# Optimization experiments

Hardware: AMD Instinct MI355X
Metric: run time of the kernel (lower is better)

Reference implementation:

```python
import jax, jax.numpy as jnp
import numpy as np
from jax import lax

CLAMP = 4.135
OUT = 7            # RoI pool output size
SCALE = 1.0 / 16.0 # feature-map stride 16


def bilinear_gather(feat, bidx, y, x):
    """feat [B,C,H,W]; bidx [N] int; y,x [N,Ph,Pw] coords in feature space -> [N,C,Ph,Pw]."""
    B, C, H, W = feat.shape
    y = jnp.clip(y, 0.0, H - 1.0)
    x = jnp.clip(x, 0.0, W - 1.0)
    y0 = jnp.floor(y); x0 = jnp.floor(x)
    y0i = y0.astype(jnp.int32); x0i = x0.astype(jnp.int32)
    y1i = jnp.minimum(y0i + 1, H - 1); x1i = jnp.minimum(x0i + 1, W - 1)
    wy1 = y - y0; wx1 = x - x0
    wy0 = 1.0 - wy1; wx0 = 1.0 - wx1
    flat = feat.transpose(0, 2, 3, 1).reshape(B * H * W, C)
    base = (bidx * (H * W))[:, None, None]
    def g(yy, xx):
        return flat[base + yy * W + xx]  # [N,Ph,Pw,C]
    out = ((wy0 * wx0)[..., None] * g(y0i, x0i)
           + (wy0 * wx1)[..., None] * g(y0i, x1i)
           + (wy1 * wx0)[..., None] * g(y1i, x0i)
           + (wy1 * wx1)[..., None] * g(y1i, x1i))
    return out.transpose(0, 3, 1, 2)


def roi_align(feat, boxes, bidx):
    """RoIAlign, sampling_ratio=1 (one bilinear sample per bin center)."""
    N = boxes.shape[0]
    b = boxes * SCALE
    x1, y1, x2, y2 = b[:, 0], b[:, 1], b[:, 2], b[:, 3]
    bw = jnp.maximum(x2 - x1, 1.0) / OUT
    bh = jnp.maximum(y2 - y1, 1.0) / OUT
    c = jnp.arange(OUT, dtype=feat.dtype) + 0.5
    ys = y1[:, None] + c * bh[:, None]   # [N,OUT]
    xs = x1[:, None] + c * bw[:, None]
    yg = jnp.broadcast_to(ys[:, :, None], (N, OUT, OUT))
    xg = jnp.broadcast_to(xs[:, None, :], (N, OUT, OUT))
    return bilinear_gather(feat, bidx, yg, xg)


def xyxy_to_rbox(b):
    cx = (b[:, 0] + b[:, 2]) * 0.5
    cy = (b[:, 1] + b[:, 3]) * 0.5
    w = b[:, 2] - b[:, 0]
    h = b[:, 3] - b[:, 1]
    return jnp.stack([cx, cy, w, h, jnp.zeros_like(cx)], axis=1)


def decode_deltas_to_rboxes(rboxes, deltas):
    cx, cy, w, h, a = (rboxes[:, i] for i in range(5))
    dx, dy, dw, dh, da = (deltas[:, i] for i in range(5))
    return jnp.stack([cx + dx * w, cy + dy * h,
                      w * jnp.exp(dw), h * jnp.exp(dh), a + da], axis=1)


def grid_sample_zeros(feat, gx, gy):
    """F.grid_sample(bilinear, padding_mode='zeros', align_corners=False).
    feat [N,C,H,W]; gx,gy [N,Ho,Wo] normalized coords -> [N,C,Ho,Wo]."""
    N, C, H, W = feat.shape
    ix = ((gx + 1.0) * W - 1.0) * 0.5
    iy = ((gy + 1.0) * H - 1.0) * 0.5
    x0 = jnp.floor(ix); y0 = jnp.floor(iy)
    wx1 = ix - x0; wy1 = iy - y0
    x0i = x0.astype(jnp.int32); y0i = y0.astype(jnp.int32)
    flat = feat.transpose(0, 2, 3, 1).reshape(N, H * W, C)
    Ho, Wo = gx.shape[1], gx.shape[2]
    def g(yy, xx, wt):
        valid = ((yy >= 0) & (yy < H) & (xx >= 0) & (xx < W)).astype(feat.dtype)
        idx = jnp.clip(yy, 0, H - 1) * W + jnp.clip(xx, 0, W - 1)
        v = jnp.take_along_axis(flat, idx.reshape(N, -1, 1), axis=1)
        v = v.reshape(N, Ho, Wo, C)
        return (wt * valid)[..., None] * v
    out = (g(y0i, x0i, (1 - wy1) * (1 - wx1))
           + g(y0i, x0i + 1, (1 - wy1) * wx1)
           + g(y0i + 1, x0i, wy1 * (1 - wx1))
           + g(y0i + 1, x0i + 1, wy1 * wx1))
    return out.transpose(0, 3, 1, 2)


def setup_inputs() -> dict:
    key = jax.random.key(0)
    ks = jax.random.split(key, 12)
    B, C, H, W = 2, 256, 64, 64
    N, NC = 2048, 16
    FD = C * OUT * OUT  # 12544
    features = jax.random.normal(ks[0], (B, C, H, W), jnp.float32)
    # valid image-space boxes (image 1024x1024, stride-16 features)
    cx = jax.random.uniform(ks[1], (N,), minval=96.0, maxval=928.0)
    cy = jax.random.uniform(ks[2], (N,), minval=96.0, maxval=928.0)
    bw = jax.random.uniform(ks[3], (N,), minval=16.0, maxval=128.0)
    bh = jax.random.uniform(ks[4], (N,), minval=16.0, maxval=128.0)
    proposals = jnp.stack([cx - bw / 2, cy - bh / 2, cx + bw / 2, cy + bh / 2], axis=1)
    batch_idx = jnp.repeat(jnp.arange(B, dtype=jnp.int32), N // B)
    s = 0.02
    return {
        "features": features,
        "proposals": proposals,
        "batch_idx": batch_idx,
        "conv_w": jax.random.normal(ks[5], (C, C, 3, 3), jnp.float32) * s,
        "conv_b": jnp.zeros((C,), jnp.float32),
        "align_w": jax.random.normal(ks[6], (5, FD), jnp.float32) * s,
        "align_b": jnp.zeros((5,), jnp.float32),
        "fc1_w": jax.random.normal(ks[7], (1024, FD), jnp.float32) * s,
        "fc1_b": jnp.zeros((1024,), jnp.float32),
        "fc2_w": jax.random.normal(ks[8], (1024, 1024), jnp.float32) * s,
        "fc2_b": jnp.zeros((1024,), jnp.float32),
        "cls_w": jax.random.normal(ks[9], (NC, 1024), jnp.float32) * s,
        "cls_b": jnp.zeros((NC,), jnp.float32),
        "box_w": jax.random.normal(ks[10], (5, 1024), jnp.float32) * s,
        "box_b": jnp.zeros((5,), jnp.float32),
    }


def reference(features, proposals, batch_idx, conv_w, conv_b, align_w, align_b,
              fc1_w, fc1_b, fc2_w, fc2_b, cls_w, cls_b, box_w, box_b):
    N = proposals.shape[0]
    # 1) RoI align
    box_feat = roi_align(features, proposals, batch_idx)           # [N,256,7,7]
    a = lax.conv_general_dilated(box_feat, conv_w, (1, 1), ((1, 1), (1, 1)),
                                 dimension_numbers=("NCHW", "OIHW", "NCHW"))
    a = jax.nn.relu(a + conv_b[None, :, None, None]).reshape(N, -1)
    coarse = jnp.clip(a @ align_w.T + align_b, -CLAMP, CLAMP)      # [N,5]
    # 3) decode to rboxes (torch.no_grad -> stop_gradient)
    prop_rb = xyxy_to_rbox(proposals)
    align_rb = lax.stop_gradient(decode_deltas_to_rboxes(prop_rb, coarse))
    # 4) affine grid from rbox (no translation, matches source) + grid_sample
    w, h, ang = align_rb[:, 2], align_rb[:, 3], align_rb[:, 4]
    cth, sth = jnp.cos(ang), jnp.sin(ang)
    sx, sy = w / OUT, h / OUT
    base = (2.0 * jnp.arange(OUT, dtype=box_feat.dtype) + 1.0) / OUT - 1.0
    xb = base[None, None, :]
    yb = base[None, :, None]
    gx = (sx * cth)[:, None, None] * xb + (-(sy * sth))[:, None, None] * yb
    gy = (sx * sth)[:, None, None] * xb + (sy * cth)[:, None, None] * yb
    aligned = grid_sample_zeros(box_feat, gx, gy)                  # [N,256,7,7]
    # 5) refine head MLP + predictors
    r = jax.nn.relu(aligned.reshape(N, -1) @ fc1_w.T + fc1_b)
    r = jax.nn.relu(r @ fc2_w.T + fc2_b)
    logits = r @ cls_w.T + cls_b                                   # [N,16]
    final = jnp.clip(r @ box_w.T + box_b, -CLAMP, CLAMP)           # [N,5]
    # 6) eval-path decode + softmax (per-class NMS is dynamic-shape postproc, excluded)
    pred_rboxes = decode_deltas_to_rboxes(prop_rb, final)
    scores = jax.nn.softmax(logits, axis=-1)
    return jnp.concatenate([pred_rboxes, scores], axis=1)          # [N,21]
```

## Files before the change

### kernel.cpp

```cpp
#include <hip/hip_runtime.h>
#include <hip/hip_bf16.h>
#include <math.h>
#include <type_traits>

constexpr int B = 2, C = 256, H = 64, W = 64, HW = H * W;
constexpr int N = 2048, OUT = 7, P = 49, FD = C * P;
constexpr int K1 = 1024;
constexpr float CLAMP_V = 4.135f, SCALE_V = 1.0f / 16.0f;
constexpr int LDB = 264;

typedef short s8v __attribute__((ext_vector_type(8)));
typedef short s4v __attribute__((ext_vector_type(4)));
typedef float f32x4 __attribute__((ext_vector_type(4)));

template <int I, int NN, class F>
__device__ __forceinline__ void static_for(F&& f) {
    if constexpr (I < NN) {
        f(std::integral_constant<int, I>{});
        static_for<I + 1, NN>(static_cast<F&&>(f));
    }
}

__device__ __forceinline__ int xcd_swz(int blk, int nblk) {
    const int cpx = nblk >> 3;
    return (blk & 7) * cpx + (blk >> 3);
}

__global__ void k_prep_all(const float* __restrict__ features, float* __restrict__ featT,
                           const float* __restrict__ conv_w, __hip_bfloat16* __restrict__ wB,
                           const float* __restrict__ align_w, float4* __restrict__ aw4,
                           float* __restrict__ aw1,
                           const float* __restrict__ fc1_w, __hip_bfloat16* __restrict__ fc1B,
                           const float* __restrict__ fc2_w, __hip_bfloat16* __restrict__ fc2B) {
    __shared__ float smem[64 * 49];
    const int id = blockIdx.x;
    const int t = threadIdx.x;
    if (id < 2048) {
        const int x = id % 128, y = (id / 128) % 8, b = id / 1024;
        const int c0 = y * 32, p0 = x * 32;
        const int tx = t % 32, ty = t / 32;
        float* tile = smem;
#pragma unroll
        for (int r = 0; r < 32; r += 8)
            tile[(ty + r) * 33 + tx] = features[(size_t)(b * C + c0 + ty + r) * HW + p0 + tx];
        __syncthreads();
#pragma unroll
        for (int r = 0; r < 32; r += 8)
            featT[(size_t)(b * HW + p0 + ty + r) * C + c0 + tx] = tile[tx * 33 + ty + r];
    } else if (id < 2120) {
        const int T = id - 2048;
        const int tap = T / 8, s = T % 8;
        const int co = t;
#pragma unroll
        for (int q = 0; q < 4; ++q)
#pragma unroll
            for (int j = 0; j < 8; ++j) {
                const int ci = s * 32 + q * 8 + j;
                wB[(((size_t)T * 256 + co) * 4 + q) * 8 + j] =
                    __float2bfloat16(conv_w[(size_t)co * 2304 + ci * 9 + tap]);
            }
    } else if (id < 2169) {
        const int o = id - 2120;
        const int co = t;
        float4 v;
        v.x = align_w[(size_t)0 * FD + co * 49 + o];
        v.y = align_w[(size_t)1 * FD + co * 49 + o];
        v.z = align_w[(size_t)2 * FD + co * 49 + o];
        v.w = align_w[(size_t)3 * FD + co * 49 + o];
        aw4[o * 256 + co] = v;
        aw1[o * 256 + co] = align_w[(size_t)4 * FD + co * 49 + o];
    } else if (id < 6265) {
        const int q = id - 2169;
        const int c0 = (q % 4) * 64;
        const int o = q / 4;
        const float* src = fc1_w + (size_t)o * FD + (size_t)c0 * 49;
        for (int i = t; i < 64 * 49; i += 256) smem[i] = src[i];
        __syncthreads();
        __hip_bfloat16* dst = fc1B + (size_t)o * FD + c0;
        for (int j = t; j < 64 * 49; j += 256) {
            const int p = j >> 6, cc = j & 63;
            dst[(size_t)p * 256 + cc] = __float2bfloat16(smem[cc * 49 + p]);
        }
    } else {
        const int bid = id - 6265;
        const int n4 = (K1 * K1) / 4;
        for (int i = bid * 256 + t; i < n4; i += 256 * 256) {
            const float4 v = reinterpret_cast<const float4*>(fc2_w)[i];
            fc2B[i * 4 + 0] = __float2bfloat16(v.x);
            fc2B[i * 4 + 1] = __float2bfloat16(v.y);
            fc2B[i * 4 + 2] = __float2bfloat16(v.z);
            fc2B[i * 4 + 3] = __float2bfloat16(v.w);
        }
    }
}

__global__ __launch_bounds__(256, 2) void k_roi_conv_grid(
    const float* __restrict__ featT, const float* __restrict__ proposals,
    const int* __restrict__ bidx, const __hip_bfloat16* __restrict__ wB,
    const float* __restrict__ conv_b, const float4* __restrict__ aw4,
    const float* __restrict__ aw1, const float* __restrict__ align_b,
    __hip_bfloat16* __restrict__ alignedOut) {
    __shared__ __align__(16) __hip_bfloat16 bfh[100 * LDB];
    __shared__ float red[64];

    const int blk = xcd_swz(blockIdx.x, 1024);
    const int t = threadIdx.x;
    const int lane = t & 63, wid = t >> 6;
    const int l15 = lane & 15;
    const int qofs = (lane >> 4) * 8;

#pragma unroll
    for (int r = 0; r < 2; ++r) {
        const int n = blk * 2 + r;
        const float px1 = proposals[n * 4 + 0] * SCALE_V, py1 = proposals[n * 4 + 1] * SCALE_V;
        const float px2 = proposals[n * 4 + 2] * SCALE_V, py2 = proposals[n * 4 + 3] * SCALE_V;
        const float bw = fmaxf(px2 - px1, 1.0f) * (1.0f / OUT);
        const float bh = fmaxf(py2 - py1, 1.0f) * (1.0f / OUT);
        const int b = bidx[n];
        const float* fb = featT + (size_t)b * HW * C;
        for (int p = wid; p < P; p += 4) {
            const int pyi = p / 7, pxi = p % 7;
            float y = py1 + (pyi + 0.5f) * bh;
            float x = px1 + (pxi + 0.5f) * bw;
            y = fminf(fmaxf(y, 0.f), (float)(H - 1));
            x = fminf(fmaxf(x, 0.f), (float)(W - 1));
            const float y0f = floorf(y), x0f = floorf(x);
            const int y0 = (int)y0f, x0 = (int)x0f;
            const int y1 = min(y0 + 1, H - 1), x1 = min(x0 + 1, W - 1);
            const float wy1 = y - y0f, wx1 = x - x0f;
            const float wy0 = 1.f - wy1, wx0 = 1.f - wx1;
            const int c4 = lane * 4;
            const float4 v00 = *reinterpret_cast<const float4*>(&fb[(size_t)(y0 * W + x0) * C + c4]);
            const float4 v01 = *reinterpret_cast<const float4*>(&fb[(size_t)(y0 * W + x1) * C + c4]);
            const float4 v10 = *reinterpret_cast<const float4*>(&fb[(size_t)(y1 * W + x0) * C + c4]);
            const float4 v11 = *reinterpret_cast<const float4*>(&fb[(size_t)(y1 * W + x1) * C + c4]);
            s4v o4;
            o4[0] = (short)__bfloat16_as_ushort(__float2bfloat16(
                        wy0 * (wx0 * v00.x + wx1 * v01.x) + wy1 * (wx0 * v10.x + wx1 * v11.x)));
            o4[1] = (short)__bfloat16_as_ushort(__float2bfloat16(
                        wy0 * (wx0 * v00.y + wx1 * v01.y) + wy1 * (wx0 * v10.y + wx1 * v11.y)));
            o4[2] = (short)__bfloat16_as_ushort(__float2bfloat16(
                        wy0 * (wx0 * v00.z + wx1 * v01.z) + wy1 * (wx0 * v10.z + wx1 * v11.z)));
            o4[3] = (short)__bfloat16_as_ushort(__float2bfloat16(
                        wy0 * (wx0 * v00.w + wx1 * v01.w) + wy1 * (wx0 * v10.w + wx1 * v11.w)));
            *reinterpret_cast<s4v*>(&bfh[(2 * p + r) * LDB + c4]) = o4;
        }
    }
    bfh[98 * LDB + t] = __float2bfloat16(0.f);
    bfh[99 * LDB + t] = __float2bfloat16(0.f);
    __syncthreads();

    const int rp = l15 & 1;
    int oyt[7], oxt[7];
    bool pval[7];
    static_for<0, 7>([&](auto MT) {
        const int p = (MT.value * 16 + l15) >> 1;
        pval[MT.value] = (p < 49);
        oyt[MT.value] = p / 7;
        oxt[MT.value] = p % 7;
    });
    int bofs[4];
    static_for<0, 4>([&](auto NT) {
        const int col = wid * 64 + NT.value * 16 + l15;
        bofs[NT.value] = col * 32 + qofs;
    });

    f32x4 acc[7][4] = {};
    for (int tap = 0; tap < 9; ++tap) {
        const int dy = tap / 3 - 1, dx = tap % 3 - 1;
        int rsel[7];
        static_for<0, 7>([&](auto MT) {
            const int iy = oyt[MT.value] + dy, ix = oxt[MT.value] + dx;
            const bool v = pval[MT.value] && ((unsigned)iy < 7u) && ((unsigned)ix < 7u);
            rsel[MT.value] = (v ? (2 * (iy * 7 + ix) + rp) : (98 + rp)) * LDB;
        });
        const __hip_bfloat16* wTap = wB + (size_t)tap * 8 * 8192;
#pragma unroll
        for (int s = 0; s < 8; ++s) {
            s8v af[7], bfr[4];
            static_for<0, 4>([&](auto NT) {
                bfr[NT.value] = *reinterpret_cast<const s8v*>(&wTap[(size_t)s * 8192 + bofs[NT.value]]);
            });
            static_for<0, 7>([&](auto MT) {
                af[MT.value] = *reinterpret_cast<const s8v*>(&bfh[rsel[MT.value] + s * 32 + qofs]);
            });
            __builtin_amdgcn_s_setprio(1);
            static_for<0, 7>([&](auto MT) {
                static_for<0, 4>([&](auto NT) {
                    acc[MT.value][NT.value] = __builtin_amdgcn_mfma_f32_16x16x32_bf16(
                        af[MT.value], bfr[NT.value], acc[MT.value][NT.value], 0, 0, 0);
                });
            });
            __builtin_amdgcn_s_setprio(0);
        }
    }

    const int hi = lane >> 4;
    float cb[4];
    static_for<0, 4>([&](auto NT) { cb[NT.value] = conv_b[wid * 64 + NT.value * 16 + l15]; });
    float pc[2][5] = {};
    static_for<0, 7>([&](auto MT) {
        static_for<0, 4>([&](auto RR) {
            constexpr int r = RR.value & 1;
            const int p = MT.value * 8 + hi * 2 + (RR.value >> 1);
            if (p < 49) {
                static_for<0, 4>([&](auto NT) {
                    const int co = wid * 64 + NT.value * 16 + l15;
                    const float4 w4 = aw4[p * 256 + co];
                    const float  w1 = aw1[p * 256 + co];
                    const float a = fmaxf(acc[MT.value][NT.value][RR.value] + cb[NT.value], 0.f);
                    pc[r][0] = fmaf(a, w4.x, pc[r][0]);
                    pc[r][1] = fmaf(a, w4.y, pc[r][1]);
                    pc[r][2] = fmaf(a, w4.z, pc[r][2]);
                    pc[r][3] = fmaf(a, w4.w, pc[r][3]);
                    pc[r][4] = fmaf(a, w1,   pc[r][4]);
                });
            }
        });
    });
    static_for<0, 2>([&](auto RI) {
        static_for<0, 5>([&](auto J) {
            float s = pc[RI.value][J.value];
#pragma unroll
            for (int off = 32; off; off >>= 1) s += __shfl_xor(s, off);
            pc[RI.value][J.value] = s;
        });
        if (lane == 0) {
            static_for<0, 5>([&](auto J) { red[RI.value * 20 + wid * 5 + J.value] = pc[RI.value][J.value]; });
        }
    });
    __syncthreads();

    if (t < 2) {
        const int r = t;
        const int n = blk * 2 + r;
        float coarse[5];
        static_for<0, 5>([&](auto Jc) {
            constexpr int j = Jc.value;
            float s = red[r * 20 + j] + red[r * 20 + 5 + j] + red[r * 20 + 10 + j] +
                      red[r * 20 + 15 + j] + align_b[j];
            coarse[j] = fminf(fmaxf(s, -CLAMP_V), CLAMP_V);
        });
        const float x1r = proposals[n * 4 + 0], y1r = proposals[n * 4 + 1];
        const float x2r = proposals[n * 4 + 2], y2r = proposals[n * 4 + 3];
        const float w = x2r - x1r, h = y2r - y1r;
        const float w2 = w * expf(coarse[2]);
        const float h2 = h * expf(coarse[3]);
        const float ang = coarse[4];
        const float cth = cosf(ang), sth = sinf(ang);
        const float sx = w2 * (1.0f / OUT), sy = h2 * (1.0f / OUT);
        red[48 + r * 4 + 0] = sx * cth;
        red[48 + r * 4 + 1] = sy * sth;
        red[48 + r * 4 + 2] = sx * sth;
        red[48 + r * 4 + 3] = sy * cth;
    }
    __syncthreads();

#pragma unroll
    for (int r = 0; r < 2; ++r) {
        const float gA = red[48 + r * 4 + 0], gBv = red[48 + r * 4 + 1];
        const float gC = red[48 + r * 4 + 2], gD = red[48 + r * 4 + 3];
        __hip_bfloat16* ao = alignedOut + (size_t)(blk * 2 + r) * FD;
        const int c4 = lane * 4;
        for (int p = wid; p < P; p += 4) {
            const int pyi = p / 7, pxi = p % 7;
            const float xb = (2 * pxi + 1) * (1.0f / OUT) - 1.0f;
            const float yb = (2 * pyi + 1) * (1.0f / OUT) - 1.0f;
            const float gx = gA * xb - gBv * yb;
            const float gy = gC * xb + gD * yb;
            const float ix = ((gx + 1.0f) * OUT - 1.0f) * 0.5f;
            const float iy = ((gy + 1.0f) * OUT - 1.0f) * 0.5f;
            const float x0f = floorf(ix), y0f = floorf(iy);
            const int x0 = (int)x0f, y0 = (int)y0f;
            const float wx1 = ix - x0f, wy1 = iy - y0f;
            const float wx0 = 1.f - wx1, wy0 = 1.f - wy1;
            const float w00 = wy0 * wx0, w01 = wy0 * wx1, w10 = wy1 * wx0, w11 = wy1 * wx1;
            const bool vx0 = (unsigned)x0 < 7u, vx1 = (unsigned)(x0 + 1) < 7u;
            const bool vy0 = (unsigned)y0 < 7u, vy1 = (unsigned)(y0 + 1) < 7u;
            const int r00 = (vy0 && vx0) ? (y0 * 7 + x0) : 49;
            const int r01 = (vy0 && vx1) ? (y0 * 7 + x0 + 1) : 49;
            const int r10 = (vy1 && vx0) ? ((y0 + 1) * 7 + x0) : 49;
            const int r11 = (vy1 && vx1) ? ((y0 + 1) * 7 + x0 + 1) : 49;
            const s4v b00 = *reinterpret_cast<const s4v*>(&bfh[(2 * r00 + r) * LDB + c4]);
            const s4v b01 = *reinterpret_cast<const s4v*>(&bfh[(2 * r01 + r) * LDB + c4]);
            const s4v b10 = *reinterpret_cast<const s4v*>(&bfh[(2 * r10 + r) * LDB + c4]);
            const s4v b11 = *reinterpret_cast<const s4v*>(&bfh[(2 * r11 + r) * LDB + c4]);
            s4v o4;
            static_for<0, 4>([&](auto J) {
                constexpr int j = J.value;
                float v = w00 * __bfloat162float(__ushort_as_bfloat16((unsigned short)b00[j]))
                        + w01 * __bfloat162float(__ushort_as_bfloat16((unsigned short)b01[j]))
                        + w10 * __bfloat162float(__ushort_as_bfloat16((unsigned short)b10[j]))
                        + w11 * __bfloat162float(__ushort_as_bfloat16((unsigned short)b11[j]));
                o4[j] = (short)__bfloat16_as_ushort(__float2bfloat16(v));
            });
            *reinterpret_cast<s4v*>(&ao[p * 256 + c4]) = o4;
        }
    }
}

template <int BM, int BN, int BK>
__global__ __launch_bounds__(256, 4) void k_gemm_bf16(
    const __hip_bfloat16* __restrict__ A, const __hip_bfloat16* __restrict__ Wt,
    const float* __restrict__ bias, float* __restrict__ CoutF,
    __hip_bfloat16* __restrict__ CoutH, int M, int Nn, int K, int relu) {
    constexpr int LD = BK + 8;
    __shared__ __align__(16) __hip_bfloat16 As[2][BM * LD];
    __shared__ __align__(16) __hip_bfloat16 Ws[2][BN * LD];
    const int ntb = Nn / BN;
    const int blkS = xcd_swz(blockIdx.x, gridDim.x);
    const int bx = blkS % ntb, by = blkS / ntb;
    const int t = threadIdx.x;
    const int lane = t & 63, wid = t >> 6;
    const int l15 = lane & 15;
    const int qofs = (lane >> 4) * 8;
    const int wm = wid >> 1, wn = wid & 1;

    const int ar = t >> 3, ak = (t & 7) * 8;
    const size_t aBase = (size_t)(by * BM) * K;
    const size_t bBase = (size_t)(bx * BN) * K;

    f32x4 acc[2][2] = {};

    const int steps = K / BK;
    {
        const s8v a0 = *reinterpret_cast<const s8v*>(&A[aBase + (size_t)ar * K + ak]);
        const s8v a1 = *reinterpret_cast<const s8v*>(&A[aBase + (size_t)(ar + 32) * K + ak]);
        const s8v b0 = *reinterpret_cast<const s8v*>(&Wt[bBase + (size_t)ar * K + ak]);
        const s8v b1 = *reinterpret_cast<const s8v*>(&Wt[bBase + (size_t)(ar + 32) * K + ak]);
        *reinterpret_cast<s8v*>(&As[0][ar * LD + ak]) = a0;
        *reinterpret_cast<s8v*>(&As[0][(ar + 32) * LD + ak]) = a1;
        *reinterpret_cast<s8v*>(&Ws[0][ar * LD + ak]) = b0;
        *reinterpret_cast<s8v*>(&Ws[0][(ar + 32) * LD + ak]) = b1;
    }
    __syncthreads();

    for (int s = 0; s < steps; ++s) {
        const int cur = s & 1;
        const bool pf = (s + 1 < steps);
        s8v a0, a1, b0, b1;
        if (pf) {
            const int k0 = (s + 1) * BK;
            a0 = *reinterpret_cast<const s8v*>(&A[aBase + (size_t)ar * K + k0 + ak]);
            a1 = *reinterpret_cast<const s8v*>(&A[aBase + (size_t)(ar + 32) * K + k0 + ak]);
            b0 = *reinterpret_cast<const s8v*>(&Wt[bBase + (size_t)ar * K + k0 + ak]);
            b1 = *reinterpret_cast<const s8v*>(&Wt[bBase + (size_t)(ar + 32) * K + k0 + ak]);
        }
        static_for<0, 2>([&](auto KH) {
            s8v afr[2], bfr[2];
            static_for<0, 2>([&](auto MT) {
                afr[MT.value] = *reinterpret_cast<const s8v*>(
                    &As[cur][(wm * 32 + MT.value * 16 + l15) * LD + KH.value * 32 + qofs]);
            });
            static_for<0, 2>([&](auto NT) {
                bfr[NT.value] = *reinterpret_cast<const s8v*>(
                    &Ws[cur][(wn * 32 + NT.value * 16 + l15) * LD + KH.value * 32 + qofs]);
            });
            static_for<0, 2>([&](auto MT) {
                static_for<0, 2>([&](auto NT) {
                    acc[MT.value][NT.value] = __builtin_amdgcn_mfma_f32_16x16x32_bf16(
                        afr[MT.value], bfr[NT.value], acc[MT.value][NT.value], 0, 0, 0);
                });
            });
        });
        if (pf) {
            __syncthreads();
            const int nxt = cur ^ 1;
            *reinterpret_cast<s8v*>(&As[nxt][ar * LD + ak]) = a0;
            *reinterpret_cast<s8v*>(&As[nxt][(ar + 32) * LD + ak]) = a1;
            *reinterpret_cast<s8v*>(&Ws[nxt][ar * LD + ak]) = b0;
            *reinterpret_cast<s8v*>(&Ws[nxt][(ar + 32) * LD + ak]) = b1;
            __syncthreads();
        }
    }

    static_for<0, 2>([&](auto MT) {
        static_for<0, 2>([&](auto NT) {
            const int col = bx * BN + wn * 32 + NT.value * 16 + l15;
            const float bv = bias[col];
            static_for<0, 4>([&](auto RR) {
                const int row = by * BM + wm * 32 + MT.value * 16 + (lane >> 4) * 4 + RR.value;
                float v = acc[MT.value][NT.value][RR.value] + bv;
                if (relu) v = fmaxf(v, 0.f);
                if (CoutF) CoutF[(size_t)row * Nn + col] = v;
                if (CoutH) CoutH[(size_t)row * Nn + col] = __float2bfloat16(v);
            });
        });
    });
}

__global__ void k_heads(const float* __restrict__ r2, const float* __restrict__ cls_w,
                        const float* __restrict__ cls_b, const float* __restrict__ box_w,
                        const float* __restrict__ box_b, const float* __restrict__ proposals,
                        float* __restrict__ out) {
    const int n = blockIdx.x;
    const int t = threadIdx.x;
    const float* r = r2 + (size_t)n * K1;
    float rv[16];
    static_for<0, 16>([&](auto Jc) { rv[Jc.value] = r[t + 64 * Jc.value]; });
    float s[21];
    static_for<0, 21>([&](auto Oc) {
        constexpr int o = Oc.value;
        const float* w = (o < 16) ? (cls_w + (size_t)o * K1) : (box_w + (size_t)(o - 16) * K1);
        float a = 0.f;
        static_for<0, 16>([&](auto Jc) { a = fmaf(rv[Jc.value], w[t + 64 * Jc.value], a); });
#pragma unroll
        for (int off = 32; off; off >>= 1) a += __shfl_xor(a, off);
        s[o] = a;
    });
    float logits[16];
    float m = -1e30f;
    static_for<0, 16>([&](auto Oc) {
        logits[Oc.value] = s[Oc.value] + cls_b[Oc.value];
        m = fmaxf(m, logits[Oc.value]);
    });
    float es = 0.f;
    static_for<0, 16>([&](auto Oc) {
        logits[Oc.value] = expf(logits[Oc.value] - m);
        es += logits[Oc.value];
    });
    const float inv = 1.0f / es;
    float fdelta[5];
    static_for<0, 5>([&](auto Jc) {
        fdelta[Jc.value] = fminf(fmaxf(s[16 + Jc.value] + box_b[Jc.value], -CLAMP_V), CLAMP_V);
    });
    const float x1r = proposals[n * 4 + 0], y1r = proposals[n * 4 + 1];
    const float x2r = proposals[n * 4 + 2], y2r = proposals[n * 4 + 3];
    const float cx = (x1r + x2r) * 0.5f, cy = (y1r + y2r) * 0.5f;
    const float w = x2r - x1r, h = y2r - y1r;
    float pred[5];
    pred[0] = cx + fdelta[0] * w;
    pred[1] = cy + fdelta[1] * h;
    pred[2] = w * expf(fdelta[2]);
    pred[3] = h * expf(fdelta[3]);
    pred[4] = fdelta[4];
    float* orow = out + (size_t)n * 21;
    static_for<0, 5>([&](auto Oc) {
        if (t == Oc.value) orow[Oc.value] = pred[Oc.value];
    });
    static_for<0, 16>([&](auto Oc) {
        if (t == 5 + Oc.value) orow[5 + Oc.value] = logits[Oc.value] * inv;
    });
}

extern "C" void kernel_launch(void* const* d_in, const int* in_sizes, int n_in,
                              void* d_out, int out_size, void* d_ws, size_t ws_size,
                              hipStream_t stream) {
    (void)in_sizes; (void)n_in; (void)out_size; (void)ws_size;
    const float* features  = (const float*)d_in[0];
    const float* proposals = (const float*)d_in[1];
    const int*   batch_idx = (const int*)d_in[2];
    const float* conv_w    = (const float*)d_in[3];
    const float* conv_b    = (const float*)d_in[4];
    const float* align_w   = (const float*)d_in[5];
    const float* align_b   = (const float*)d_in[6];
    const float* fc1_w     = (const float*)d_in[7];
    const float* fc1_b     = (const float*)d_in[8];
    const float* fc2_w     = (const float*)d_in[9];
    const float* fc2_b     = (const float*)d_in[10];
    const float* cls_w     = (const float*)d_in[11];
    const float* cls_b     = (const float*)d_in[12];
    const float* box_w     = (const float*)d_in[13];
    const float* box_b     = (const float*)d_in[14];
    float* out = (float*)d_out;

    float* ws    = (float*)d_ws;
    float* featT = ws;
    float* r2    = featT + (size_t)B * HW * C;
    float4* aw4  = (float4*)(r2 + (size_t)N * K1);
    float* aw1   = (float*)(aw4 + 49 * 256);
    __hip_bfloat16* alignedH = (__hip_bfloat16*)(aw1 + 49 * 256);
    __hip_bfloat16* r1H   = alignedH + (size_t)N * FD;
    __hip_bfloat16* wB    = r1H + (size_t)N * K1;
    __hip_bfloat16* fc1B  = wB + 2304 * 256;
    __hip_bfloat16* fc2B  = fc1B + (size_t)K1 * FD;

    k_prep_all<<<6521, 256, 0, stream>>>(features, featT, conv_w, wB, align_w, aw4, aw1,
                                         fc1_w, fc1B, fc2_w, fc2B);
    k_roi_conv_grid<<<N / 2, 256, 0, stream>>>(featT, proposals, batch_idx, wB, conv_b,
                                               aw4, aw1, align_b, alignedH);
    k_gemm_bf16<64, 64, 64><<<(N / 64) * (K1 / 64), 256, 0, stream>>>(
        alignedH, fc1B, fc1_b, nullptr, r1H, N, K1, FD, 1);
    k_gemm_bf16<64, 64, 64><<<(N / 64) * (K1 / 64), 256, 0, stream>>>(
        r1H, fc2B, fc2_b, r2, nullptr, N, K1, K1, 1);
    k_heads<<<N, 64, 0, stream>>>(r2, cls_w, cls_b, box_w, box_b, proposals, out);
}
```

Before: 305.7 us.

## Process one RoI per block in fused RoI-align/conv/grid-sample kernel

Each block of the fused RoI kernel now handles a single proposal instead of two interleaved ones. The conv GEMM uses 4 M-tiles (64 rows covering 49 positions) instead of 7 tiles over 98 interleaved rows, and the launch bounds are dropped. LDS use and accumulator registers shrink, which should raise occupancy. In exchange, each conv weight fragment loaded from global memory is reused across one RoI instead of two, doubling weight traffic, and padding waste rises from 98/112 to 49/64 useful rows.

```diff
diff --git a/kernel.cpp b/kernel.cpp
--- a/kernel.cpp
+++ b/kernel.cpp
@@ -94,24 +94,22 @@
     }
 }
 
-__global__ __launch_bounds__(256, 2) void k_roi_conv_grid(
+__global__ void k_roi_conv_grid(
     const float* __restrict__ featT, const float* __restrict__ proposals,
     const int* __restrict__ bidx, const __hip_bfloat16* __restrict__ wB,
     const float* __restrict__ conv_b, const float4* __restrict__ aw4,
     const float* __restrict__ aw1, const float* __restrict__ align_b,
     __hip_bfloat16* __restrict__ alignedOut) {
-    __shared__ __align__(16) __hip_bfloat16 bfh[100 * LDB];
-    __shared__ float red[64];
-
-    const int blk = xcd_swz(blockIdx.x, 1024);
+    __shared__ __align__(16) __hip_bfloat16 bfh[50 * LDB];
+    __shared__ float red[44];
+
+    const int n = xcd_swz(blockIdx.x, 2048);
     const int t = threadIdx.x;
     const int lane = t & 63, wid = t >> 6;
     const int l15 = lane & 15;
     const int qofs = (lane >> 4) * 8;
 
-#pragma unroll
-    for (int r = 0; r < 2; ++r) {
-        const int n = blk * 2 + r;
+    {
         const float px1 = proposals[n * 4 + 0] * SCALE_V, py1 = proposals[n * 4 + 1] * SCALE_V;
         const float px2 = proposals[n * 4 + 2] * SCALE_V, py2 = proposals[n * 4 + 3] * SCALE_V;
         const float bw = fmaxf(px2 - px1, 1.0f) * (1.0f / OUT);
@@ -143,18 +141,16 @@
                         wy0 * (wx0 * v00.z + wx1 * v01.z) + wy1 * (wx0 * v10.z + wx1 * v11.z)));
             o4[3] = (short)__bfloat16_as_ushort(__float2bfloat16(
                         wy0 * (wx0 * v00.w + wx1 * v01.w) + wy1 * (wx0 * v10.w + wx1 * v11.w)));
-            *reinterpret_cast<s4v*>(&bfh[(2 * p + r) * LDB + c4]) = o4;
-        }
-    }
-    bfh[98 * LDB + t] = __float2bfloat16(0.f);
-    bfh[99 * LDB + t] = __float2bfloat16(0.f);
+            *reinterpret_cast<s4v*>(&bfh[p * LDB + c4]) = o4;
+        }
+    }
+    bfh[49 * LDB + t] = __float2bfloat16(0.f);
     __syncthreads();
 
-    const int rp = l15 & 1;
-    int oyt[7], oxt[7];
-    bool pval[7];
-    static_for<0, 7>([&](auto MT) {
-        const int p = (MT.value * 16 + l15) >> 1;
+    int oyt[4], oxt[4];
+    bool pval[4];
+    static_for<0, 4>([&](auto MT) {
+        const int p = MT.value * 16 + l15;
         pval[MT.value] = (p < 49);
         oyt[MT.value] = p / 7;
         oxt[MT.value] = p % 7;
@@ -165,27 +161,27 @@
         bofs[NT.value] = col * 32 + qofs;
     });
 
-    f32x4 acc[7][4] = {};
+    f32x4 acc[4][4] = {};
     for (int tap = 0; tap < 9; ++tap) {
         const int dy = tap / 3 - 1, dx = tap % 3 - 1;
-        int rsel[7];
-        static_for<0, 7>([&](auto MT) {
+        int rsel[4];
+        static_for<0, 4>([&](auto MT) {
             const int iy = oyt[MT.value] + dy, ix = oxt[MT.value] + dx;
             const bool v = pval[MT.value] && ((unsigned)iy < 7u) && ((unsigned)ix < 7u);
-            rsel[MT.value] = (v ? (2 * (iy * 7 + ix) + rp) : (98 + rp)) * LDB;
+            rsel[MT.value] = (v ? (iy * 7 + ix) : 49) * LDB;
         });
         const __hip_bfloat16* wTap = wB + (size_t)tap * 8 * 8192;
 #pragma unroll
         for (int s = 0; s < 8; ++s) {
-            s8v af[7], bfr[4];
+            s8v af[4], bfr[4];
             static_for<0, 4>([&](auto NT) {
                 bfr[NT.value] = *reinterpret_cast<const s8v*>(&wTap[(size_t)s * 8192 + bofs[NT.value]]);
             });
-            static_for<0, 7>([&](auto MT) {
+            static_for<0, 4>([&](auto MT) {
                 af[MT.value] = *reinterpret_cast<const s8v*>(&bfh[rsel[MT.value] + s * 32 + qofs]);
             });
             __builtin_amdgcn_s_setprio(1);
-            static_for<0, 7>([&](auto MT) {
+            static_for<0, 4>([&](auto MT) {
                 static_for<0, 4>([&](auto NT) {
                     acc[MT.value][NT.value] = __builtin_amdgcn_mfma_f32_16x16x32_bf16(
                         af[MT.value], bfr[NT.value], acc[MT.value][NT.value], 0, 0, 0);
@@ -198,47 +194,41 @@
     const int hi = lane >> 4;
     float cb[4];
     static_for<0, 4>([&](auto NT) { cb[NT.value] = conv_b[wid * 64 + NT.value * 16 + l15]; });
-    float pc[2][5] = {};
-    static_for<0, 7>([&](auto MT) {
+    float pc[5] = {};
+    static_for<0, 4>([&](auto MT) {
         static_for<0, 4>([&](auto RR) {
-            constexpr int r = RR.value & 1;
-            const int p = MT.value * 8 + hi * 2 + (RR.value >> 1);
-            if (p < 49) {
+            const int o = MT.value * 16 + hi * 4 + RR.value;
+            if (o < 49) {
                 static_for<0, 4>([&](auto NT) {
                     const int co = wid * 64 + NT.value * 16 + l15;
-                    const float4 w4 = aw4[p * 256 + co];
-                    const float  w1 = aw1[p * 256 + co];
+                    const float4 w4 = aw4[o * 256 + co];
+                    const float  w1 = aw1[o * 256 + co];
                     const float a = fmaxf(acc[MT.value][NT.value][RR.value] + cb[NT.value], 0.f);
-                    pc[r][0] = fmaf(a, w4.x, pc[r][0]);
-                    pc[r][1] = fmaf(a, w4.y, pc[r][1]);
-                    pc[r][2] = fmaf(a, w4.z, pc[r][2]);
-                    pc[r][3] = fmaf(a, w4.w, pc[r][3]);
-                    pc[r][4] = fmaf(a, w1,   pc[r][4]);
+                    pc[0] = fmaf(a, w4.x, pc[0]);
+                    pc[1] = fmaf(a, w4.y, pc[1]);
+                    pc[2] = fmaf(a, w4.z, pc[2]);
+                    pc[3] = fmaf(a, w4.w, pc[3]);
+                    pc[4] = fmaf(a, w1,   pc[4]);
                 });
             }
         });
     });
-    static_for<0, 2>([&](auto RI) {
-        static_for<0, 5>([&](auto J) {
-            float s = pc[RI.value][J.value];
-#pragma unroll
-            for (int off = 32; off; off >>= 1) s += __shfl_xor(s, off);
-            pc[RI.value][J.value] = s;
-        });
-        if (lane == 0) {
-            static_for<0, 5>([&](auto J) { red[RI.value * 20 + wid * 5 + J.value] = pc[RI.value][J.value]; });
-        }
-    });
+    static_for<0, 5>([&](auto J) {
+        float s = pc[J.value];
+#pragma unroll
+        for (int off = 32; off; off >>= 1) s += __shfl_xor(s, off);
+        pc[J.value] = s;
+    });
+    if (lane == 0) {
+        static_for<0, 5>([&](auto J) { red[wid * 5 + J.value] = pc[J.value]; });
+    }
     __syncthreads();
 
-    if (t < 2) {
-        const int r = t;
-        const int n = blk * 2 + r;
+    if (t == 0) {
         float coarse[5];
         static_for<0, 5>([&](auto Jc) {
             constexpr int j = Jc.value;
-            float s = red[r * 20 + j] + red[r * 20 + 5 + j] + red[r * 20 + 10 + j] +
-                      red[r * 20 + 15 + j] + align_b[j];
+            float s = red[j] + red[5 + j] + red[10 + j] + red[15 + j] + align_b[j];
             coarse[j] = fminf(fmaxf(s, -CLAMP_V), CLAMP_V);
         });
         const float x1r = proposals[n * 4 + 0], y1r = proposals[n * 4 + 1];
@@ -249,18 +239,16 @@
         const float ang = coarse[4];
         const float cth = cosf(ang), sth = sinf(ang);
         const float sx = w2 * (1.0f / OUT), sy = h2 * (1.0f / OUT);
-        red[48 + r * 4 + 0] = sx * cth;
-        red[48 + r * 4 + 1] = sy * sth;
-        red[48 + r * 4 + 2] = sx * sth;
-        red[48 + r * 4 + 3] = sy * cth;
+        red[40] = sx * cth;
+        red[41] = sy * sth;
+        red[42] = sx * sth;
+        red[43] = sy * cth;
     }
     __syncthreads();
 
-#pragma unroll
-    for (int r = 0; r < 2; ++r) {
-        const float gA = red[48 + r * 4 + 0], gBv = red[48 + r * 4 + 1];
-        const float gC = red[48 + r * 4 + 2], gD = red[48 + r * 4 + 3];
-        __hip_bfloat16* ao = alignedOut + (size_t)(blk * 2 + r) * FD;
+    {
+        const float gA = red[40], gBv = red[41], gC = red[42], gD = red[43];
+        __hip_bfloat16* ao = alignedOut + (size_t)n * FD;
         const int c4 = lane * 4;
         for (int p = wid; p < P; p += 4) {
             const int pyi = p / 7, pxi = p % 7;
@@ -281,10 +269,10 @@
             const int r01 = (vy0 && vx1) ? (y0 * 7 + x0 + 1) : 49;
             const int r10 = (vy1 && vx0) ? ((y0 + 1) * 7 + x0) : 49;
             const int r11 = (vy1 && vx1) ? ((y0 + 1) * 7 + x0 + 1) : 49;
-            const s4v b00 = *reinterpret_cast<const s4v*>(&bfh[(2 * r00 + r) * LDB + c4]);
-            const s4v b01 = *reinterpret_cast<const s4v*>(&bfh[(2 * r01 + r) * LDB + c4]);
-            const s4v b10 = *reinterpret_cast<const s4v*>(&bfh[(2 * r10 + r) * LDB + c4]);
-            const s4v b11 = *reinterpret_cast<const s4v*>(&bfh[(2 * r11 + r) * LDB + c4]);
+            const s4v b00 = *reinterpret_cast<const s4v*>(&bfh[r00 * LDB + c4]);
+            const s4v b01 = *reinterpret_cast<const s4v*>(&bfh[r01 * LDB + c4]);
+            const s4v b10 = *reinterpret_cast<const s4v*>(&bfh[r10 * LDB + c4]);
+            const s4v b11 = *reinterpret_cast<const s4v*>(&bfh[r11 * LDB + c4]);
             s4v o4;
             static_for<0, 4>([&](auto J) {
                 constexpr int j = J.value;
@@ -477,8 +465,8 @@
 
     k_prep_all<<<6521, 256, 0, stream>>>(features, featT, conv_w, wB, align_w, aw4, aw1,
                                          fc1_w, fc1B, fc2_w, fc2B);
-    k_roi_conv_grid<<<N / 2, 256, 0, stream>>>(featT, proposals, batch_idx, wB, conv_b,
-                                               aw4, aw1, align_b, alignedH);
+    k_roi_conv_grid<<<N, 256, 0, stream>>>(featT, proposals, batch_idx, wB, conv_b,
+                                           aw4, aw1, align_b, alignedH);
     k_gemm_bf16<64, 64, 64><<<(N / 64) * (K1 / 64), 256, 0, stream>>>(
         alignedH, fc1B, fc1_b, nullptr, r1H, N, K1, FD, 1);
     k_gemm_bf16<64, 64, 64><<<(N / 64) * (K1 / 64), 256, 0, stream>>>(
```

Result: slower. 346.5 us (+13.3%).
